# Performance work log

Measured on AMD Instinct MI355X. Metric: run time of the kernel, lower is better.

Reference implementation:

```python
import jax, jax.numpy as jnp
import numpy as np

DIM = 512
NUM_HEADS = 8
HEAD_DIM = DIM // NUM_HEADS
SCALE = HEAD_DIM ** -0.5


def setup_inputs() -> dict:
    key = jax.random.key(0)
    ks = jax.random.split(key, 5)
    B, N = 4, 2048
    x = jax.random.normal(ks[0], (B, N, DIM), dtype=jnp.float32)
    # Learned parameters (torch nn.Linear style: y = x @ W.T + b)
    w_qkv = jax.random.normal(ks[1], (3 * DIM, DIM), dtype=jnp.float32) * (DIM ** -0.5)
    b_qkv = jnp.zeros((3 * DIM,), dtype=jnp.float32)
    w_proj = jax.random.normal(ks[2], (DIM, DIM), dtype=jnp.float32) * (DIM ** -0.5)
    b_proj = jnp.zeros((DIM,), dtype=jnp.float32)
    return {"x": x, "w_qkv": w_qkv, "b_qkv": b_qkv, "w_proj": w_proj, "b_proj": b_proj}


def reference(x, w_qkv, b_qkv, w_proj, b_proj):
    B, N, C = x.shape
    qkv = x @ w_qkv.T + b_qkv                      # [B, N, 3C]
    qkv = qkv.reshape(B, N, 3, NUM_HEADS, HEAD_DIM)
    qkv = jnp.transpose(qkv, (2, 0, 3, 1, 4))      # [3, B, H, N, d]
    q, k, v = qkv[0], qkv[1], qkv[2]
    attn = jnp.einsum("bhqd,bhkd->bhqk", q, k) * SCALE  # [B, H, N, N]
    attn = jax.nn.softmax(attn, axis=-1)
    out = jnp.einsum("bhqk,bhkd->bhqd", attn, v)   # [B, H, N, d]
    out = jnp.transpose(out, (0, 2, 1, 3)).reshape(B, N, C)
    return out @ w_proj.T + b_proj
```

## Files before the change

kernel.cpp:

```cpp
#include <hip/hip_runtime.h>

#define DIM 512
#define NHEAD 8
#define HDIM 64
#define BATCH 4
#define SEQ 2048
#define MTOT (BATCH*SEQ)
#define SCALE 0.125f
#define LOG2E 1.4426950408889634f

typedef __bf16 bf16_t;
typedef __bf16 bf16x8 __attribute__((ext_vector_type(8)));
typedef __bf16 bf16x4 __attribute__((ext_vector_type(4)));
typedef float f32x4 __attribute__((ext_vector_type(4)));

#define ASYNC_COPY16(g, l) __builtin_amdgcn_global_load_lds( \
    (const __attribute__((address_space(1))) void*)(g),      \
    (__attribute__((address_space(3))) void*)(l), 16, 0, 0)

#define NX_ELEM  (4194304)
#define NWQ_ELEM (786432)
#define NWP_ELEM (262144)
__global__ __launch_bounds__(256) void cvt_kernel(const float* __restrict__ x,
                                                  const float* __restrict__ wq,
                                                  const float* __restrict__ wp,
                                                  bf16_t* __restrict__ out) {
    int i = (blockIdx.x * 256 + threadIdx.x) * 4;
    const float* src;
    if (i < NX_ELEM)                 src = x  + i;
    else if (i < NX_ELEM + NWQ_ELEM) src = wq + (i - NX_ELEM);
    else                             src = wp + (i - NX_ELEM - NWQ_ELEM);
    float4 v = *reinterpret_cast<const float4*>(src);
    bf16x4 o;
    o[0] = (bf16_t)v.x; o[1] = (bf16_t)v.y; o[2] = (bf16_t)v.z; o[3] = (bf16_t)v.w;
    *reinterpret_cast<bf16x4*>(out + i) = o;
}

__global__ __launch_bounds__(256) void gemm_qkv_kernel(
    const bf16_t* __restrict__ X, const bf16_t* __restrict__ W,
    const float* __restrict__ bias,
    bf16_t* __restrict__ Qo, bf16_t* __restrict__ Ko, bf16_t* __restrict__ Vto)
{
    __shared__ bf16_t As[128][64];
    __shared__ bf16_t Bs[128][64];
    const int tid = threadIdx.x;
    const int wave = tid >> 6, lane = tid & 63;
    const int lhi = lane >> 4, llo = lane & 15;
    const int o = blockIdx.x;
    const int x = o & 7, i0 = o >> 3;
    const int m0 = (x * 8 + (i0 & 7)) * 128;
    const int n0 = (i0 >> 3) * 128;
    const int wr = (wave >> 1) * 64, wc = (wave & 1) * 64;
    f32x4 acc[4][4] = {};

    const int srow = wave * 32 + (lane >> 3);
    const int scol = (lane & 7) * 8;
    const bf16_t* gA = X + (size_t)(m0 + srow) * DIM + scol;
    const bf16_t* gB = W + (size_t)(n0 + srow) * DIM + scol;

    for (int k0 = 0; k0 < DIM; k0 += 64) {
        #pragma unroll
        for (int p = 0; p < 4; ++p) {
            ASYNC_COPY16(gA + (size_t)p * 8 * DIM + k0, &As[wave*32 + p*8][0]);
            ASYNC_COPY16(gB + (size_t)p * 8 * DIM + k0, &Bs[wave*32 + p*8][0]);
        }
        __syncthreads();
        #pragma unroll
        for (int ks = 0; ks < 2; ++ks) {
            bf16x8 af[4], bfr[4];
            #pragma unroll
            for (int i = 0; i < 4; ++i)
                af[i] = *reinterpret_cast<const bf16x8*>(&As[wr + i*16 + llo][ks*32 + lhi*8]);
            #pragma unroll
            for (int j = 0; j < 4; ++j)
                bfr[j] = *reinterpret_cast<const bf16x8*>(&Bs[wc + j*16 + llo][ks*32 + lhi*8]);
            __builtin_amdgcn_s_setprio(1);
            #pragma unroll
            for (int i = 0; i < 4; ++i)
                #pragma unroll
                for (int j = 0; j < 4; ++j)
                    acc[i][j] = __builtin_amdgcn_mfma_f32_16x16x32_bf16(af[i], bfr[j], acc[i][j], 0, 0, 0);
            __builtin_amdgcn_s_setprio(0);
        }
        __syncthreads();
    }

    #pragma unroll
    for (int j = 0; j < 4; ++j) {
        int col = n0 + wc + j*16 + llo;
        int which = col >> 9;
        int hh = (col >> 6) & 7;
        int dd = col & 63;
        float bv = bias[col];
        #pragma unroll
        for (int i = 0; i < 4; ++i) {
            #pragma unroll
            for (int r = 0; r < 4; ++r) {
                int m = m0 + wr + i*16 + lhi*4 + r;
                int b = m >> 11, ns = m & 2047;
                float v = acc[i][j][r] + bv;
                size_t bh = (size_t)(b * NHEAD + hh);
                if (which == 0)
                    Qo[(bh * SEQ + ns) * HDIM + dd] = (bf16_t)(v * (SCALE * LOG2E));
                else if (which == 1)
                    Ko[(bh * SEQ + ns) * HDIM + dd] = (bf16_t)v;
                else
                    Vto[(bh * HDIM + dd) * SEQ + ns] = (bf16_t)v;
            }
        }
    }
}

__global__ __launch_bounds__(256, 4) void attn_kernel(
    const bf16_t* __restrict__ Q, const bf16_t* __restrict__ K,
    const bf16_t* __restrict__ Vt, bf16_t* __restrict__ O)
{
    __shared__ bf16_t Ks[2][128][72];
    __shared__ bf16_t Vs[2][64][136];
    const int tid = threadIdx.x;
    const int wave = tid >> 6, lane = tid & 63;
    const int lhi = lane >> 4, llo = lane & 15;
    const int o = blockIdx.x;
    const int w = (o & 7) * 64 + (o >> 3);
    const int qt = w & 15, bh = w >> 4;
    const bf16_t* Qb = Q + (size_t)bh * SEQ * HDIM;
    const bf16_t* Kb = K + (size_t)bh * SEQ * HDIM;
    const bf16_t* Vb = Vt + (size_t)bh * HDIM * SEQ;
    const int q0 = qt * 128 + wave * 32;

    const int ksr = tid >> 3, kscc = (tid & 7) * 8;
    const int vd = tid >> 4, vg = tid & 15;
    auto pk_first  = [](int g) { return 32*(g>>2) + 8*((2*g)&3)   + 4*((g>>1)&1); };
    auto pk_second = [](int g) { return 32*(g>>2) + 8*((2*g+1)&3) + 4*((g>>1)&1); };
    const int pkA = pk_first(vg), pkB = pk_second(vg);

    bf16x8 aq[2][2];
    #pragma unroll
    for (int qb = 0; qb < 2; ++qb)
        #pragma unroll
        for (int ks = 0; ks < 2; ++ks)
            aq[qb][ks] = *reinterpret_cast<const bf16x8*>(
                Qb + (size_t)(q0 + qb*16 + llo) * HDIM + ks*32 + lhi*8);

    f32x4 acc_o[2][4] = {};
    float mstat[2], lstat[2];
    mstat[0] = mstat[1] = -1e30f;
    lstat[0] = lstat[1] = 0.f;
    const float THR = 8.0f * LOG2E;

    uint4 kreg[4], vreg[4];
    #pragma unroll
    for (int r = 0; r < 4; ++r) {
        kreg[r] = *reinterpret_cast<const uint4*>(Kb + (size_t)(ksr + r*32) * HDIM + kscc);
        vreg[r] = *reinterpret_cast<const uint4*>(Vb + (size_t)(vd + r*16) * SEQ + vg*8);
    }
    #pragma unroll
    for (int r = 0; r < 4; ++r) {
        *reinterpret_cast<uint4*>(&Ks[0][ksr + r*32][kscc]) = kreg[r];
        *reinterpret_cast<uint2*>(&Vs[0][vd + r*16][pkA]) = make_uint2(vreg[r].x, vreg[r].y);
        *reinterpret_cast<uint2*>(&Vs[0][vd + r*16][pkB]) = make_uint2(vreg[r].z, vreg[r].w);
    }
    __syncthreads();

    const int NT = SEQ / 128;
    for (int kt = 0; kt < NT; ++kt) {
        const int cur = kt & 1, nxt = cur ^ 1;

        if (kt + 1 < NT) {
            const size_t koff = (size_t)(kt + 1) * 128;
            #pragma unroll
            for (int r = 0; r < 4; ++r) {
                kreg[r] = *reinterpret_cast<const uint4*>(Kb + (koff + ksr + r*32) * HDIM + kscc);
                vreg[r] = *reinterpret_cast<const uint4*>(Vb + (size_t)(vd + r*16) * SEQ + koff + vg*8);
            }
        }

        f32x4 s[2][8];
        #pragma unroll
        for (int qb = 0; qb < 2; ++qb)
            #pragma unroll
            for (int kb = 0; kb < 8; ++kb) s[qb][kb] = f32x4{0.f, 0.f, 0.f, 0.f};
        __builtin_amdgcn_s_setprio(1);
        #pragma unroll
        for (int kb = 0; kb < 8; ++kb) {
            #pragma unroll
            for (int ks = 0; ks < 2; ++ks) {
                bf16x8 kf = *reinterpret_cast<const bf16x8*>(&Ks[cur][kb*16 + llo][ks*32 + lhi*8]);
                #pragma unroll
                for (int qb = 0; qb < 2; ++qb)
                    s[qb][kb] = __builtin_amdgcn_mfma_f32_16x16x32_bf16(kf, aq[qb][ks], s[qb][kb], 0, 0, 0);
            }
        }
        __builtin_amdgcn_s_setprio(0);

        float lmax[2];
        bool ok = true;
        #pragma unroll
        for (int qb = 0; qb < 2; ++qb) {
            float mx = s[qb][0][0];
            #pragma unroll
            for (int kb = 0; kb < 8; ++kb)
                #pragma unroll
                for (int r = 0; r < 4; ++r) mx = fmaxf(mx, s[qb][kb][r]);
            lmax[qb] = mx;
            ok &= (mx <= mstat[qb] + THR);
        }

        if (!__all(ok)) {
            #pragma unroll
            for (int qb = 0; qb < 2; ++qb) {
                float mx = lmax[qb];
                mx = fmaxf(mx, __shfl_xor(mx, 16, 64));
                mx = fmaxf(mx, __shfl_xor(mx, 32, 64));
                float mold = mstat[qb];
                float mn = fmaxf(mold, mx);
                float alpha = __builtin_amdgcn_exp2f(mold - mn);
                mstat[qb] = mn;
                lstat[qb] *= alpha;
                #pragma unroll
                for (int r = 0; r < 4; ++r) {
                    float av = __shfl(alpha, (lane & 48) >> 2 | r, 64);
                    #pragma unroll
                    for (int db = 0; db < 4; ++db) acc_o[qb][db][r] *= av;
                }
            }
        }

        float rs[2] = {0.f, 0.f};
        #pragma unroll
        for (int kp = 0; kp < 4; ++kp) {
            bf16x8 ap[2];
            #pragma unroll
            for (int qb = 0; qb < 2; ++qb) {
                #pragma unroll
                for (int j = 0; j < 4; ++j) {
                    float p0 = __builtin_amdgcn_exp2f(s[qb][2*kp][j]     - mstat[qb]);
                    float p1 = __builtin_amdgcn_exp2f(s[qb][2*kp + 1][j] - mstat[qb]);
                    rs[qb] += p0 + p1;
                    ap[qb][j]     = (bf16_t)p0;
                    ap[qb][4 + j] = (bf16_t)p1;
                }
            }
            __builtin_amdgcn_s_setprio(1);
            #pragma unroll
            for (int db = 0; db < 4; ++db) {
                bf16x8 bv = *reinterpret_cast<const bf16x8*>(&Vs[cur][db*16 + llo][kp*32 + lhi*8]);
                #pragma unroll
                for (int qb = 0; qb < 2; ++qb)
                    acc_o[qb][db] = __builtin_amdgcn_mfma_f32_16x16x32_bf16(ap[qb], bv, acc_o[qb][db], 0, 0, 0);
            }
            __builtin_amdgcn_s_setprio(0);
        }
        #pragma unroll
        for (int qb = 0; qb < 2; ++qb) {
            float r = rs[qb];
            r += __shfl_xor(r, 16, 64);
            r += __shfl_xor(r, 32, 64);
            lstat[qb] += r;
        }

        if (kt + 1 < NT) {
            #pragma unroll
            for (int r = 0; r < 4; ++r) {
                *reinterpret_cast<uint4*>(&Ks[nxt][ksr + r*32][kscc]) = kreg[r];
                *reinterpret_cast<uint2*>(&Vs[nxt][vd + r*16][pkA]) = make_uint2(vreg[r].x, vreg[r].y);
                *reinterpret_cast<uint2*>(&Vs[nxt][vd + r*16][pkB]) = make_uint2(vreg[r].z, vreg[r].w);
            }
        }
        __syncthreads();
    }

    const int b = bh >> 3, h = bh & 7;
    #pragma unroll
    for (int qb = 0; qb < 2; ++qb) {
        float inv = 1.0f / lstat[qb];
        #pragma unroll
        for (int r = 0; r < 4; ++r) {
            float iv = __shfl(inv, (lane & 48) >> 2 | r, 64);
            int q = q0 + qb*16 + lhi*4 + r;
            #pragma unroll
            for (int db = 0; db < 4; ++db)
                O[(size_t)(b * SEQ + q) * DIM + h*HDIM + db*16 + llo] =
                    (bf16_t)(acc_o[qb][db][r] * iv);
        }
    }
}

__global__ __launch_bounds__(256) void gemm_proj_kernel(
    const bf16_t* __restrict__ X, const bf16_t* __restrict__ W,
    const float* __restrict__ bias, float* __restrict__ out)
{
    __shared__ bf16_t As[128][64];
    __shared__ bf16_t Bs[128][64];
    const int tid = threadIdx.x;
    const int wave = tid >> 6, lane = tid & 63;
    const int lhi = lane >> 4, llo = lane & 15;
    const int o = blockIdx.x;
    const int x = o & 7, i0 = o >> 3;
    const int m0 = (x * 8 + (i0 & 7)) * 128;
    const int n0 = (i0 >> 3) * 128;
    const int wr = (wave >> 1) * 64, wc = (wave & 1) * 64;
    f32x4 acc[4][4] = {};

    const int srow = wave * 32 + (lane >> 3);
    const int scol = (lane & 7) * 8;
    const bf16_t* gA = X + (size_t)(m0 + srow) * DIM + scol;
    const bf16_t* gB = W + (size_t)(n0 + srow) * DIM + scol;

    for (int k0 = 0; k0 < DIM; k0 += 64) {
        #pragma unroll
        for (int p = 0; p < 4; ++p) {
            ASYNC_COPY16(gA + (size_t)p * 8 * DIM + k0, &As[wave*32 + p*8][0]);
            ASYNC_COPY16(gB + (size_t)p * 8 * DIM + k0, &Bs[wave*32 + p*8][0]);
        }
        __syncthreads();
        #pragma unroll
        for (int ks = 0; ks < 2; ++ks) {
            bf16x8 af[4], bfr[4];
            #pragma unroll
            for (int i = 0; i < 4; ++i)
                af[i] = *reinterpret_cast<const bf16x8*>(&As[wr + i*16 + llo][ks*32 + lhi*8]);
            #pragma unroll
            for (int j = 0; j < 4; ++j)
                bfr[j] = *reinterpret_cast<const bf16x8*>(&Bs[wc + j*16 + llo][ks*32 + lhi*8]);
            __builtin_amdgcn_s_setprio(1);
            #pragma unroll
            for (int i = 0; i < 4; ++i)
                #pragma unroll
                for (int j = 0; j < 4; ++j)
                    acc[i][j] = __builtin_amdgcn_mfma_f32_16x16x32_bf16(af[i], bfr[j], acc[i][j], 0, 0, 0);
            __builtin_amdgcn_s_setprio(0);
        }
        __syncthreads();
    }

    #pragma unroll
    for (int j = 0; j < 4; ++j) {
        int col = n0 + wc + j*16 + llo;
        float bv = bias[col];
        #pragma unroll
        for (int i = 0; i < 4; ++i)
            #pragma unroll
            for (int r = 0; r < 4; ++r) {
                int m = m0 + wr + i*16 + lhi*4 + r;
                out[(size_t)m * DIM + col] = acc[i][j][r] + bv;
            }
    }
}

extern "C" void kernel_launch(void* const* d_in, const int* in_sizes, int n_in,
                              void* d_out, int out_size, void* d_ws, size_t ws_size,
                              hipStream_t stream) {
    const float* x      = (const float*)d_in[0];
    const float* w_qkv  = (const float*)d_in[1];
    const float* b_qkv  = (const float*)d_in[2];
    const float* w_proj = (const float*)d_in[3];
    const float* b_proj = (const float*)d_in[4];
    float* out = (float*)d_out;

    const size_t NX  = (size_t)MTOT * DIM;
    const size_t NWQ = (size_t)3 * DIM * DIM;
    const size_t NWP = (size_t)DIM * DIM;
    const size_t NQ  = (size_t)BATCH * NHEAD * SEQ * HDIM;

    bf16_t* Xb    = (bf16_t*)d_ws;
    bf16_t* Wqkv  = Xb + NX;
    bf16_t* Wproj = Wqkv + NWQ;
    bf16_t* Qb    = Wproj + NWP;
    bf16_t* Kb    = Qb + NQ;
    bf16_t* Vtb   = Kb + NQ;
    bf16_t* AOb   = Vtb + NQ;

    cvt_kernel<<<(int)((NX + NWQ + NWP) / 1024), 256, 0, stream>>>(x, w_qkv, w_proj, Xb);

    gemm_qkv_kernel<<<768, 256, 0, stream>>>(Xb, Wqkv, b_qkv, Qb, Kb, Vtb);

    attn_kernel<<<512, 256, 0, stream>>>(Qb, Kb, Vtb, AOb);

    gemm_proj_kernel<<<256, 256, 0, stream>>>(AOb, Wproj, b_proj, out);
}
```

Measured before the change: 97.01 us.

## Load K/V fragments directly from global into registers, dropping LDS staging

The attention kernel no longer stages K and V tiles through double-buffered shared memory with block-wide barriers. Each wave now reads its MFMA operand fragments straight from global memory (K prefetched one tile ahead, V loaded per 64-key tile), and the key tile shrinks from 128 to 64. Launch bounds drop to 2 blocks per CU. This removes LDS writes, LDS reads and __syncthreads, but each of the four waves in a block now fetches the same K/V data separately from global memory/L2, using narrower uncoalesced-ish loads and more registers.

```diff
diff --git a/kernel.cpp b/kernel.cpp
--- a/kernel.cpp
+++ b/kernel.cpp
@@ -111,12 +111,10 @@
     }
 }
 
-__global__ __launch_bounds__(256, 4) void attn_kernel(
+__global__ __launch_bounds__(256, 2) void attn_kernel(
     const bf16_t* __restrict__ Q, const bf16_t* __restrict__ K,
     const bf16_t* __restrict__ Vt, bf16_t* __restrict__ O)
 {
-    __shared__ bf16_t Ks[2][128][72];
-    __shared__ bf16_t Vs[2][64][136];
     const int tid = threadIdx.x;
     const int wave = tid >> 6, lane = tid & 63;
     const int lhi = lane >> 4, llo = lane & 15;
@@ -128,12 +126,6 @@
     const bf16_t* Vb = Vt + (size_t)bh * HDIM * SEQ;
     const int q0 = qt * 128 + wave * 32;
 
-    const int ksr = tid >> 3, kscc = (tid & 7) * 8;
-    const int vd = tid >> 4, vg = tid & 15;
-    auto pk_first  = [](int g) { return 32*(g>>2) + 8*((2*g)&3)   + 4*((g>>1)&1); };
-    auto pk_second = [](int g) { return 32*(g>>2) + 8*((2*g+1)&3) + 4*((g>>1)&1); };
-    const int pkA = pk_first(vg), pkB = pk_second(vg);
-
     bf16x8 aq[2][2];
     #pragma unroll
     for (int qb = 0; qb < 2; ++qb)
@@ -148,50 +140,50 @@
     lstat[0] = lstat[1] = 0.f;
     const float THR = 8.0f * LOG2E;
 
-    uint4 kreg[4], vreg[4];
-    #pragma unroll
-    for (int r = 0; r < 4; ++r) {
-        kreg[r] = *reinterpret_cast<const uint4*>(Kb + (size_t)(ksr + r*32) * HDIM + kscc);
-        vreg[r] = *reinterpret_cast<const uint4*>(Vb + (size_t)(vd + r*16) * SEQ + vg*8);
-    }
-    #pragma unroll
-    for (int r = 0; r < 4; ++r) {
-        *reinterpret_cast<uint4*>(&Ks[0][ksr + r*32][kscc]) = kreg[r];
-        *reinterpret_cast<uint2*>(&Vs[0][vd + r*16][pkA]) = make_uint2(vreg[r].x, vreg[r].y);
-        *reinterpret_cast<uint2*>(&Vs[0][vd + r*16][pkB]) = make_uint2(vreg[r].z, vreg[r].w);
-    }
-    __syncthreads();
-
-    const int NT = SEQ / 128;
+    const bf16_t* kbase = Kb + (size_t)llo * HDIM + lhi * 8;
+    const bf16_t* vbase = Vb + (size_t)llo * SEQ + lhi * 4;
+
+    bf16x8 kf[4][2];
+    #pragma unroll
+    for (int kb = 0; kb < 4; ++kb)
+        #pragma unroll
+        for (int ks = 0; ks < 2; ++ks)
+            kf[kb][ks] = *reinterpret_cast<const bf16x8*>(
+                kbase + (size_t)(kb*16) * HDIM + ks*32);
+
+    const int NT = SEQ / 64;
     for (int kt = 0; kt < NT; ++kt) {
-        const int cur = kt & 1, nxt = cur ^ 1;
+        const int koff = kt * 64;
+
+        uint2 vf[2][4][2];
+        #pragma unroll
+        for (int kp = 0; kp < 2; ++kp)
+            #pragma unroll
+            for (int db = 0; db < 4; ++db)
+                #pragma unroll
+                for (int c = 0; c < 2; ++c)
+                    vf[kp][db][c] = *reinterpret_cast<const uint2*>(
+                        vbase + (size_t)(db*16) * SEQ + koff + kp*32 + c*16);
+
+        f32x4 s[2][4] = {};
+        __builtin_amdgcn_s_setprio(1);
+        #pragma unroll
+        for (int kb = 0; kb < 4; ++kb)
+            #pragma unroll
+            for (int ks = 0; ks < 2; ++ks)
+                #pragma unroll
+                for (int qb = 0; qb < 2; ++qb)
+                    s[qb][kb] = __builtin_amdgcn_mfma_f32_16x16x32_bf16(kf[kb][ks], aq[qb][ks], s[qb][kb], 0, 0, 0);
+        __builtin_amdgcn_s_setprio(0);
 
         if (kt + 1 < NT) {
-            const size_t koff = (size_t)(kt + 1) * 128;
-            #pragma unroll
-            for (int r = 0; r < 4; ++r) {
-                kreg[r] = *reinterpret_cast<const uint4*>(Kb + (koff + ksr + r*32) * HDIM + kscc);
-                vreg[r] = *reinterpret_cast<const uint4*>(Vb + (size_t)(vd + r*16) * SEQ + koff + vg*8);
-            }
-        }
-
-        f32x4 s[2][8];
-        #pragma unroll
-        for (int qb = 0; qb < 2; ++qb)
-            #pragma unroll
-            for (int kb = 0; kb < 8; ++kb) s[qb][kb] = f32x4{0.f, 0.f, 0.f, 0.f};
-        __builtin_amdgcn_s_setprio(1);
-        #pragma unroll
-        for (int kb = 0; kb < 8; ++kb) {
-            #pragma unroll
-            for (int ks = 0; ks < 2; ++ks) {
-                bf16x8 kf = *reinterpret_cast<const bf16x8*>(&Ks[cur][kb*16 + llo][ks*32 + lhi*8]);
-                #pragma unroll
-                for (int qb = 0; qb < 2; ++qb)
-                    s[qb][kb] = __builtin_amdgcn_mfma_f32_16x16x32_bf16(kf, aq[qb][ks], s[qb][kb], 0, 0, 0);
-            }
-        }
-        __builtin_amdgcn_s_setprio(0);
+            #pragma unroll
+            for (int kb = 0; kb < 4; ++kb)
+                #pragma unroll
+                for (int ks = 0; ks < 2; ++ks)
+                    kf[kb][ks] = *reinterpret_cast<const bf16x8*>(
+                        kbase + (size_t)(koff + 64 + kb*16) * HDIM + ks*32);
+        }
 
         float lmax[2];
         bool ok = true;
@@ -199,7 +191,7 @@
         for (int qb = 0; qb < 2; ++qb) {
             float mx = s[qb][0][0];
             #pragma unroll
-            for (int kb = 0; kb < 8; ++kb)
+            for (int kb = 0; kb < 4; ++kb)
                 #pragma unroll
                 for (int r = 0; r < 4; ++r) mx = fmaxf(mx, s[qb][kb][r]);
             lmax[qb] = mx;
@@ -226,48 +218,46 @@
             }
         }
 
-        float rs[2] = {0.f, 0.f};
-        #pragma unroll
-        for (int kp = 0; kp < 4; ++kp) {
+        #pragma unroll
+        for (int qb = 0; qb < 2; ++qb) {
+            float rs = 0.f;
+            #pragma unroll
+            for (int kb = 0; kb < 4; ++kb)
+                #pragma unroll
+                for (int r = 0; r < 4; ++r) {
+                    float pv = __builtin_amdgcn_exp2f(s[qb][kb][r] - mstat[qb]);
+                    s[qb][kb][r] = pv;
+                    rs += pv;
+                }
+            rs += __shfl_xor(rs, 16, 64);
+            rs += __shfl_xor(rs, 32, 64);
+            lstat[qb] += rs;
+        }
+
+        #pragma unroll
+        for (int kp = 0; kp < 2; ++kp) {
             bf16x8 ap[2];
             #pragma unroll
-            for (int qb = 0; qb < 2; ++qb) {
+            for (int qb = 0; qb < 2; ++qb)
                 #pragma unroll
                 for (int j = 0; j < 4; ++j) {
-                    float p0 = __builtin_amdgcn_exp2f(s[qb][2*kp][j]     - mstat[qb]);
-                    float p1 = __builtin_amdgcn_exp2f(s[qb][2*kp + 1][j] - mstat[qb]);
-                    rs[qb] += p0 + p1;
-                    ap[qb][j]     = (bf16_t)p0;
-                    ap[qb][4 + j] = (bf16_t)p1;
+                    ap[qb][j]     = (bf16_t)s[qb][2*kp][j];
+                    ap[qb][4 + j] = (bf16_t)s[qb][2*kp + 1][j];
                 }
-            }
             __builtin_amdgcn_s_setprio(1);
             #pragma unroll
             for (int db = 0; db < 4; ++db) {
-                bf16x8 bv = *reinterpret_cast<const bf16x8*>(&Vs[cur][db*16 + llo][kp*32 + lhi*8]);
+                bf16x4 l0 = *reinterpret_cast<const bf16x4*>(&vf[kp][db][0]);
+                bf16x4 l1 = *reinterpret_cast<const bf16x4*>(&vf[kp][db][1]);
+                bf16x8 bv;
+                #pragma unroll
+                for (int j = 0; j < 4; ++j) { bv[j] = l0[j]; bv[4 + j] = l1[j]; }
                 #pragma unroll
                 for (int qb = 0; qb < 2; ++qb)
                     acc_o[qb][db] = __builtin_amdgcn_mfma_f32_16x16x32_bf16(ap[qb], bv, acc_o[qb][db], 0, 0, 0);
             }
             __builtin_amdgcn_s_setprio(0);
         }
-        #pragma unroll
-        for (int qb = 0; qb < 2; ++qb) {
-            float r = rs[qb];
-            r += __shfl_xor(r, 16, 64);
-            r += __shfl_xor(r, 32, 64);
-            lstat[qb] += r;
-        }
-
-        if (kt + 1 < NT) {
-            #pragma unroll
-            for (int r = 0; r < 4; ++r) {
-                *reinterpret_cast<uint4*>(&Ks[nxt][ksr + r*32][kscc]) = kreg[r];
-                *reinterpret_cast<uint2*>(&Vs[nxt][vd + r*16][pkA]) = make_uint2(vreg[r].x, vreg[r].y);
-                *reinterpret_cast<uint2*>(&Vs[nxt][vd + r*16][pkB]) = make_uint2(vreg[r].z, vreg[r].w);
-            }
-        }
-        __syncthreads();
     }
 
     const int b = bh >> 3, h = bh & 7;
```

Result: slower. 221.9 us (+128.7%).

## Use 512-thread attention blocks with 64-key tiles and XOR-swizzled LDS

Applied to the files above, without the earlier changes.

The attention kernel now runs 8 waves per block covering 256 queries, so each loaded K/V tile is shared by twice as many queries. The key tile shrinks from 128 to 64 rows and each thread loads one vector per tile. Padded shared-memory layouts are replaced by XOR swizzling to avoid bank conflicts. In exchange the kernel runs twice as many loop iterations with more barriers, launches only 256 blocks (one per CU on a 256-CU part), and drops the occupancy hint of 4 blocks per CU.

```diff
diff --git a/kernel.cpp b/kernel.cpp
--- a/kernel.cpp
+++ b/kernel.cpp
@@ -111,28 +111,28 @@
     }
 }
 
-__global__ __launch_bounds__(256, 4) void attn_kernel(
+__global__ __launch_bounds__(512) void attn_kernel(
     const bf16_t* __restrict__ Q, const bf16_t* __restrict__ K,
     const bf16_t* __restrict__ Vt, bf16_t* __restrict__ O)
 {
-    __shared__ bf16_t Ks[2][128][72];
-    __shared__ bf16_t Vs[2][64][136];
+    __shared__ bf16_t Ks[2][64][64];
+    __shared__ bf16_t Vs[2][64][64];
     const int tid = threadIdx.x;
     const int wave = tid >> 6, lane = tid & 63;
     const int lhi = lane >> 4, llo = lane & 15;
     const int o = blockIdx.x;
-    const int w = (o & 7) * 64 + (o >> 3);
-    const int qt = w & 15, bh = w >> 4;
+    const int w = (o & 7) * 32 + (o >> 3);
+    const int qt = w & 7, bh = w >> 3;
     const bf16_t* Qb = Q + (size_t)bh * SEQ * HDIM;
     const bf16_t* Kb = K + (size_t)bh * SEQ * HDIM;
     const bf16_t* Vb = Vt + (size_t)bh * HDIM * SEQ;
-    const int q0 = qt * 128 + wave * 32;
-
-    const int ksr = tid >> 3, kscc = (tid & 7) * 8;
-    const int vd = tid >> 4, vg = tid & 15;
-    auto pk_first  = [](int g) { return 32*(g>>2) + 8*((2*g)&3)   + 4*((g>>1)&1); };
-    auto pk_second = [](int g) { return 32*(g>>2) + 8*((2*g+1)&3) + 4*((g>>1)&1); };
-    const int pkA = pk_first(vg), pkB = pk_second(vg);
+    const int q0 = qt * 256 + wave * 32;
+
+    const int ksr = tid >> 3, kg = tid & 7;
+    const int kcol = (kg * 8) ^ ((ksr & 7) * 8);
+    const int vd = tid >> 3, vg = tid & 7;
+    const int pkA = (32*(vg>>2) + 8*((2*vg)&3)   + 4*((vg>>1)&1)) ^ ((vd & 7) * 8);
+    const int pkB = (32*(vg>>2) + 8*((2*vg+1)&3) + 4*((vg>>1)&1)) ^ ((vd & 7) * 8);
 
     bf16x8 aq[2][2];
     #pragma unroll
@@ -148,44 +148,32 @@
     lstat[0] = lstat[1] = 0.f;
     const float THR = 8.0f * LOG2E;
 
-    uint4 kreg[4], vreg[4];
-    #pragma unroll
-    for (int r = 0; r < 4; ++r) {
-        kreg[r] = *reinterpret_cast<const uint4*>(Kb + (size_t)(ksr + r*32) * HDIM + kscc);
-        vreg[r] = *reinterpret_cast<const uint4*>(Vb + (size_t)(vd + r*16) * SEQ + vg*8);
-    }
-    #pragma unroll
-    for (int r = 0; r < 4; ++r) {
-        *reinterpret_cast<uint4*>(&Ks[0][ksr + r*32][kscc]) = kreg[r];
-        *reinterpret_cast<uint2*>(&Vs[0][vd + r*16][pkA]) = make_uint2(vreg[r].x, vreg[r].y);
-        *reinterpret_cast<uint2*>(&Vs[0][vd + r*16][pkB]) = make_uint2(vreg[r].z, vreg[r].w);
-    }
+    uint4 kreg, vreg;
+    kreg = *reinterpret_cast<const uint4*>(Kb + (size_t)ksr * HDIM + kg*8);
+    vreg = *reinterpret_cast<const uint4*>(Vb + (size_t)vd * SEQ + vg*8);
+    *reinterpret_cast<uint4*>(&Ks[0][ksr][kcol]) = kreg;
+    *reinterpret_cast<uint2*>(&Vs[0][vd][pkA]) = make_uint2(vreg.x, vreg.y);
+    *reinterpret_cast<uint2*>(&Vs[0][vd][pkB]) = make_uint2(vreg.z, vreg.w);
     __syncthreads();
 
-    const int NT = SEQ / 128;
+    const int NT = SEQ / 64;
     for (int kt = 0; kt < NT; ++kt) {
         const int cur = kt & 1, nxt = cur ^ 1;
 
         if (kt + 1 < NT) {
-            const size_t koff = (size_t)(kt + 1) * 128;
-            #pragma unroll
-            for (int r = 0; r < 4; ++r) {
-                kreg[r] = *reinterpret_cast<const uint4*>(Kb + (koff + ksr + r*32) * HDIM + kscc);
-                vreg[r] = *reinterpret_cast<const uint4*>(Vb + (size_t)(vd + r*16) * SEQ + koff + vg*8);
-            }
-        }
-
-        f32x4 s[2][8];
-        #pragma unroll
-        for (int qb = 0; qb < 2; ++qb)
-            #pragma unroll
-            for (int kb = 0; kb < 8; ++kb) s[qb][kb] = f32x4{0.f, 0.f, 0.f, 0.f};
+            const size_t koff = (size_t)(kt + 1) * 64;
+            kreg = *reinterpret_cast<const uint4*>(Kb + (koff + ksr) * HDIM + kg*8);
+            vreg = *reinterpret_cast<const uint4*>(Vb + (size_t)vd * SEQ + koff + vg*8);
+        }
+
+        f32x4 s[2][4] = {};
         __builtin_amdgcn_s_setprio(1);
         #pragma unroll
-        for (int kb = 0; kb < 8; ++kb) {
+        for (int kb = 0; kb < 4; ++kb) {
             #pragma unroll
             for (int ks = 0; ks < 2; ++ks) {
-                bf16x8 kf = *reinterpret_cast<const bf16x8*>(&Ks[cur][kb*16 + llo][ks*32 + lhi*8]);
+                bf16x8 kf = *reinterpret_cast<const bf16x8*>(
+                    &Ks[cur][kb*16 + llo][(ks*32 + lhi*8) ^ ((llo & 7) * 8)]);
                 #pragma unroll
                 for (int qb = 0; qb < 2; ++qb)
                     s[qb][kb] = __builtin_amdgcn_mfma_f32_16x16x32_bf16(kf, aq[qb][ks], s[qb][kb], 0, 0, 0);
@@ -199,7 +187,7 @@
         for (int qb = 0; qb < 2; ++qb) {
             float mx = s[qb][0][0];
             #pragma unroll
-            for (int kb = 0; kb < 8; ++kb)
+            for (int kb = 0; kb < 4; ++kb)
                 #pragma unroll
                 for (int r = 0; r < 4; ++r) mx = fmaxf(mx, s[qb][kb][r]);
             lmax[qb] = mx;
@@ -228,7 +216,7 @@
 
         float rs[2] = {0.f, 0.f};
         #pragma unroll
-        for (int kp = 0; kp < 4; ++kp) {
+        for (int kp = 0; kp < 2; ++kp) {
             bf16x8 ap[2];
             #pragma unroll
             for (int qb = 0; qb < 2; ++qb) {
@@ -244,7 +232,8 @@
             __builtin_amdgcn_s_setprio(1);
             #pragma unroll
             for (int db = 0; db < 4; ++db) {
-                bf16x8 bv = *reinterpret_cast<const bf16x8*>(&Vs[cur][db*16 + llo][kp*32 + lhi*8]);
+                bf16x8 bv = *reinterpret_cast<const bf16x8*>(
+                    &Vs[cur][db*16 + llo][(kp*32 + lhi*8) ^ ((llo & 7) * 8)]);
                 #pragma unroll
                 for (int qb = 0; qb < 2; ++qb)
                     acc_o[qb][db] = __builtin_amdgcn_mfma_f32_16x16x32_bf16(ap[qb], bv, acc_o[qb][db], 0, 0, 0);
@@ -260,12 +249,9 @@
         }
 
         if (kt + 1 < NT) {
-            #pragma unroll
-            for (int r = 0; r < 4; ++r) {
-                *reinterpret_cast<uint4*>(&Ks[nxt][ksr + r*32][kscc]) = kreg[r];
-                *reinterpret_cast<uint2*>(&Vs[nxt][vd + r*16][pkA]) = make_uint2(vreg[r].x, vreg[r].y);
-                *reinterpret_cast<uint2*>(&Vs[nxt][vd + r*16][pkB]) = make_uint2(vreg[r].z, vreg[r].w);
-            }
+            *reinterpret_cast<uint4*>(&Ks[nxt][ksr][kcol]) = kreg;
+            *reinterpret_cast<uint2*>(&Vs[nxt][vd][pkA]) = make_uint2(vreg.x, vreg.y);
+            *reinterpret_cast<uint2*>(&Vs[nxt][vd][pkB]) = make_uint2(vreg.z, vreg.w);
         }
         __syncthreads();
     }
@@ -375,7 +361,7 @@
 
     gemm_qkv_kernel<<<768, 256, 0, stream>>>(Xb, Wqkv, b_qkv, Qb, Kb, Vtb);
 
-    attn_kernel<<<512, 256, 0, stream>>>(Qb, Kb, Vtb, AOb);
+    attn_kernel<<<256, 512, 0, stream>>>(Qb, Kb, Vtb, AOb);
 
     gemm_proj_kernel<<<256, 256, 0, stream>>>(AOb, Wproj, b_proj, out);
 }
```

Result: faster. 93.64 us (-3.5%).
